# Kernel optimization log

Hardware: AMD Instinct MI355X
Metric: run time of the kernel (lower is better)

## Reference

```python
import jax, jax.numpy as jnp
import numpy as np

K = 7  # local_kernel_size


def conv2d(x, w, b, pad):
    # x: [B,C,H,W], w: [O,I,kh,kw]
    y = jax.lax.conv_general_dilated(
        x, w, window_strides=(1, 1), padding=[(pad, pad), (pad, pad)],
        dimension_numbers=("NCHW", "OIHW", "NCHW"))
    return y + b[None, :, None, None]


def kernel_normalize(kernel, k):
    # kernel: [B, k*k, H, W]; zero-mean over tap dim, then add 1/(k*k)
    km = jnp.mean(kernel, axis=1, keepdims=True)
    return kernel - km + 1.0 / (k * k)


def local_conv_feat(img, kernel, k):
    # Fused dynamic local conv: avoids materializing [B,C,k*k,H,W].
    # Tap order matches F.unfold row-major (dy, dx).
    B, C, H, W = img.shape
    pad = (k - 1) // 2
    imgp = jnp.pad(img, ((0, 0), (0, 0), (pad, pad), (pad, pad)))
    out = jnp.zeros_like(img)
    for dy in range(k):
        for dx in range(k):
            idx = dy * k + dx
            out = out + imgp[:, :, dy:dy + H, dx:dx + W] * kernel[:, idx:idx + 1]
    return out


def setup_inputs() -> dict:
    key = jax.random.key(0)
    ks = jax.random.split(key, 14)
    B, C, H, W = 4, 64, 128, 128
    w = lambda k, shape: jax.random.normal(k, shape, jnp.float32) * 0.05
    return {
        "x": jax.random.normal(ks[0], (B, C, H, W), jnp.float32),
        "kernel_features": jax.random.normal(ks[1], (B, C, H, W), jnp.float32),
        # feature_path: two 3x3 convs
        "fw1": w(ks[2], (C, C, 3, 3)), "fb1": jnp.zeros((C,), jnp.float32),
        "fw2": w(ks[3], (C, C, 3, 3)), "fb2": jnp.zeros((C,), jnp.float32),
        # multiplicative_path: two 3x3 convs
        "mw1": w(ks[4], (C, C, 3, 3)), "mb1": jnp.zeros((C,), jnp.float32),
        "mw2": w(ks[5], (C, C, 3, 3)), "mb2": jnp.zeros((C,), jnp.float32),
        # local_filter_path: two 1x1 convs, last outputs k*k channels
        "lw1": w(ks[6], (C, C, 1, 1)), "lb1": jnp.zeros((C,), jnp.float32),
        "lw2": w(ks[7], (K * K, C, 1, 1)), "lb2": jnp.zeros((K * K,), jnp.float32),
    }


def reference(x, kernel_features, fw1, fb1, fw2, fb2, mw1, mb1, mw2, mb2, lw1, lb1, lw2, lb2):
    # feature_path: ReLU -> conv3x3 -> ReLU -> conv3x3
    fp = conv2d(jax.nn.relu(conv2d(jax.nn.relu(x), fw1, fb1, 1)), fw2, fb2, 1)
    # multiplicative_path: conv3x3 -> ReLU -> conv3x3
    mp = conv2d(jax.nn.relu(conv2d(kernel_features, mw1, mb1, 1)), mw2, mb2, 1)
    # local_filter_path: conv1x1 -> ReLU -> conv1x1 (-> k*k channels)
    lp = conv2d(jax.nn.relu(conv2d(kernel_features, lw1, lb1, 0)), lw2, lb2, 0)
    lp = kernel_normalize(lp, K)
    feat = fp * mp
    filtered = local_conv_feat(feat, lp, K)
    return x + filtered
```

## Files before the change

### kernel.cpp

```cpp
#include <hip/hip_runtime.h>
#include <hip/hip_bf16.h>

#define Cc 64
#define Hc 128
#define Wc 128
#define HWc (Hc * Wc)
#define Bc 4

typedef __attribute__((ext_vector_type(8))) short short8;
typedef __attribute__((ext_vector_type(4))) float float4v;

static __device__ __forceinline__ unsigned short f2bu(float f) {
    __hip_bfloat16 h = __float2bfloat16(f);
    return *(unsigned short*)&h;
}

static __device__ __forceinline__ void gl_lds16(const void* g, void* l) {
    __builtin_amdgcn_global_load_lds(
        (const __attribute__((address_space(1))) unsigned int*)g,
        (__attribute__((address_space(3))) unsigned int*)l, 16, 0, 0);
}

__global__ __launch_bounds__(256) void prep_k(
    const float* __restrict__ x, const float* __restrict__ kf,
    const float* __restrict__ fw1, const float* __restrict__ fw2,
    const float* __restrict__ mw1, const float* __restrict__ mw2,
    const float* __restrict__ lw1, const float* __restrict__ lw2,
    unsigned short* __restrict__ xb, unsigned short* __restrict__ kfb,
    unsigned short* __restrict__ wbase)
{
    const int bid = blockIdx.x;
    const int tid = threadIdx.x;

    if (bid < 512) {
        const bool isx = bid < 256;
        const float* src = isx ? x : kf;
        unsigned short* dst = isx ? xb : kfb;
        const int px = (isx ? bid : bid - 256) * 256 + tid;
        const int b  = px >> 14;
        const int hw = px & 16383;
        const float* s = src + (size_t)b * Cc * HWc + hw;
        unsigned short* d = dst + (size_t)px * Cc;
#pragma unroll
        for (int c8 = 0; c8 < 8; ++c8) {
            unsigned int pk[4];
#pragma unroll
            for (int jp = 0; jp < 4; ++jp) {
                float v0 = s[(size_t)(c8 * 8 + jp * 2 + 0) * HWc];
                float v1 = s[(size_t)(c8 * 8 + jp * 2 + 1) * HWc];
                if (isx) { v0 = fmaxf(v0, 0.f); v1 = fmaxf(v1, 0.f); }
                pk[jp] = (unsigned int)f2bu(v0) | ((unsigned int)f2bu(v1) << 16);
            }
            *(uint4*)(d + c8 * 8) = make_uint4(pk[0], pk[1], pk[2], pk[3]);
        }
    } else if (bid < 584) {
        const int wbid  = bid - 512;
        const int which = wbid / 18;
        const float* w = (which == 0) ? fw1 : (which == 1) ? fw2 : (which == 2) ? mw1 : mw2;
        unsigned short* wb = wbase + (size_t)which * 36864;
        const int g = (wbid % 18) * 256 + tid;
        if (g >= 4608) return;
        const int lane = g & 63;
        const int smt  = g >> 6;
        const int s    = smt >> 2;
        const int mt   = smt & 3;
        const int co   = mt * 16 + (lane & 15);
        const int kb   = s * 32 + (lane >> 4) * 8;
        unsigned int pk[4];
#pragma unroll
        for (int jp = 0; jp < 4; ++jp) {
            int k0 = kb + jp * 2, k1 = k0 + 1;
            float v0 = w[((size_t)co * Cc + (k0 & 63)) * 9 + (k0 >> 6)];
            float v1 = w[((size_t)co * Cc + (k1 & 63)) * 9 + (k1 >> 6)];
            pk[jp] = (unsigned int)f2bu(v0) | ((unsigned int)f2bu(v1) << 16);
        }
        *(uint4*)(wb + (size_t)g * 8) = make_uint4(pk[0], pk[1], pk[2], pk[3]);
    } else {
        const int wbid  = bid - 584;
        const int which = wbid >> 1;
        const float* w = which ? lw2 : lw1;
        const int Cout = which ? 49 : 64;
        unsigned short* wb = wbase + 4 * 36864 + (size_t)which * 4096;
        const int g = (wbid & 1) * 256 + tid;
        const int lane = g & 63;
        const int smt  = g >> 6;
        const int s    = smt >> 2;
        const int mt   = smt & 3;
        const int co   = mt * 16 + (lane & 15);
        const int kb   = s * 32 + (lane >> 4) * 8;
        unsigned int pk[4];
#pragma unroll
        for (int jp = 0; jp < 4; ++jp) {
            int k0 = kb + jp * 2, k1 = k0 + 1;
            float v0 = (co < Cout) ? w[(size_t)co * Cc + k0] : 0.f;
            float v1 = (co < Cout) ? w[(size_t)co * Cc + k1] : 0.f;
            pk[jp] = (unsigned int)f2bu(v0) | ((unsigned int)f2bu(v1) << 16);
        }
        *(uint4*)(wb + (size_t)g * 8) = make_uint4(pk[0], pk[1], pk[2], pk[3]);
    }
}

#define STAGE_DMA(INPTR, SBUF)                                                \
    for (int k = wv; k < 33; k += 4) {                                        \
        const int u_  = k * 8 + (lane >> 3);                                  \
        const int j_  = lane & 7;                                             \
        const int r_  = u_ / 66;                                              \
        const int c_  = u_ - r_ * 66;                                         \
        const int gh_ = h0 - 1 + r_;                                          \
        const int gw_ = w0 - 1 + c_;                                          \
        const bool ok_ = ((unsigned)gh_ < (unsigned)Hc) && ((unsigned)gw_ < (unsigned)Wc); \
        const int ch_ = j_ ^ (u_ & 7);                                        \
        const unsigned short* g_ = ok_                                        \
            ? (INPTR) + ((((size_t)b * Hc + gh_) * Wc + gw_) << 6) + (ch_ << 3) \
            : zpage + (ch_ << 3);                                             \
        gl_lds16(g_, &(SBUF)[k * 512]);                                       \
    }

#define LOAD_A(W, s, m) (*(const short8*)((W) + (size_t)(s) * 2048 + (size_t)(m) * 512))
#define LOAD_B(SB, s, nt) ({                                                  \
        const int tap_ = (s) >> 1;                                            \
        const int qb_  = rowb[tap_ / 3] + tap_ % 3;                           \
        const int ch0_ = ((s) & 1) * 4 + quad;                                \
        *(const short8*)&(SB)[(qb_ + (nt) * 16) * 64 + ((ch0_ ^ (qb_ & 7)) << 3)]; })

#define CONV_GEMM(APTR, ACC, SB)                                              \
    {                                                                         \
        short8 a_cur[2], b_cur[4];                                            \
        _Pragma("unroll")                                                     \
        for (int m = 0; m < 2; ++m) a_cur[m] = LOAD_A(APTR, 0, m);            \
        _Pragma("unroll")                                                     \
        for (int nt = 0; nt < 4; ++nt) b_cur[nt] = LOAD_B(SB, 0, nt);         \
        _Pragma("unroll")                                                     \
        for (int s = 0; s < 18; ++s) {                                        \
            short8 a_nxt[2], b_nxt[4];                                        \
            if (s < 17) {                                                     \
                _Pragma("unroll")                                             \
                for (int m = 0; m < 2; ++m) a_nxt[m] = LOAD_A(APTR, s + 1, m);\
                _Pragma("unroll")                                             \
                for (int nt = 0; nt < 4; ++nt) b_nxt[nt] = LOAD_B(SB, s + 1, nt); \
            }                                                                 \
            _Pragma("unroll")                                                 \
            for (int nt = 0; nt < 4; ++nt)                                    \
                _Pragma("unroll")                                             \
                for (int m = 0; m < 2; ++m)                                   \
                    ACC[m][nt] = __builtin_amdgcn_mfma_f32_16x16x32_bf16(     \
                        a_cur[m], b_cur[nt], ACC[m][nt], 0, 0, 0);            \
            if (s < 17) {                                                     \
                _Pragma("unroll")                                             \
                for (int m = 0; m < 2; ++m) a_cur[m] = a_nxt[m];              \
                _Pragma("unroll")                                             \
                for (int nt = 0; nt < 4; ++nt) b_cur[nt] = b_nxt[nt];         \
            }                                                                 \
        }                                                                     \
    }

__global__ __launch_bounds__(256) void conv1_dual_k(
    const unsigned short* __restrict__ in0,
    const unsigned short* __restrict__ in1,
    const unsigned short* __restrict__ wfrag0,
    const unsigned short* __restrict__ wfrag1,
    const float* __restrict__ bias0,
    const float* __restrict__ bias1,
    const unsigned short* __restrict__ zpage,
    unsigned short* __restrict__ out0,
    unsigned short* __restrict__ out1)
{
    __shared__ unsigned short s_b[264 * 64];

    const int tid  = threadIdx.x;
    const int lane = tid & 63;
    const int wv   = tid >> 6;
    const int w0   = blockIdx.x * 64;
    const int h0   = blockIdx.y * 2;
    const int zz   = blockIdx.z;
    const int b    = zz & 3;
    const bool sel = zz >> 2;

    const unsigned short* in    = sel ? in1 : in0;
    const unsigned short* wfrag = sel ? wfrag1 : wfrag0;
    const float*          bias  = sel ? bias1 : bias0;
    unsigned short*       out   = sel ? out1 : out0;

    STAGE_DMA(in, s_b);
    __syncthreads();

    const int rowsel = wv >> 1;
    const int cohalf = wv & 1;
    const int quad   = lane >> 4;
    const int n15    = lane & 15;
    const unsigned short* aptr = wfrag + (((size_t)(cohalf * 2) * 64 + lane) << 3);

    int rowb[3];
#pragma unroll
    for (int ky = 0; ky < 3; ++ky) rowb[ky] = (rowsel + ky) * 66 + n15;

    float4v acc[2][4];
#pragma unroll
    for (int m = 0; m < 2; ++m)
#pragma unroll
        for (int nt = 0; nt < 4; ++nt) acc[m][nt] = (float4v){0.f, 0.f, 0.f, 0.f};

    CONV_GEMM(aptr, acc, s_b);

    const int h = h0 + rowsel;
#pragma unroll
    for (int m = 0; m < 2; ++m) {
        const int mt  = cohalf * 2 + m;
        const int co0 = mt * 16 + quad * 4;
        float4 bv = *(const float4*)&bias[co0];
#pragma unroll
        for (int nt = 0; nt < 4; ++nt) {
            const size_t pix = ((size_t)b * Hc + h) * Wc + w0 + nt * 16 + n15;
            ushort4 pk;
            pk.x = f2bu(fmaxf(acc[m][nt][0] + bv.x, 0.f));
            pk.y = f2bu(fmaxf(acc[m][nt][1] + bv.y, 0.f));
            pk.z = f2bu(fmaxf(acc[m][nt][2] + bv.z, 0.f));
            pk.w = f2bu(fmaxf(acc[m][nt][3] + bv.w, 0.f));
            *(ushort4*)&out[pix * Cc + co0] = pk;
        }
    }
}

__global__ __launch_bounds__(256) void conv2_fused_k(
    const unsigned short* __restrict__ t1f,
    const unsigned short* __restrict__ t1m,
    const unsigned short* __restrict__ wf,
    const unsigned short* __restrict__ wm,
    const float* __restrict__ bf,
    const float* __restrict__ bm,
    const unsigned short* __restrict__ zpage,
    float* __restrict__ feat)
{
    __shared__ unsigned short s_b2[2][264 * 64];

    const int tid  = threadIdx.x;
    const int lane = tid & 63;
    const int wv   = tid >> 6;
    const int w0   = blockIdx.x * 64;
    const int h0   = blockIdx.y * 2;
    const int b    = blockIdx.z;

    STAGE_DMA(t1f, s_b2[0]);
    STAGE_DMA(t1m, s_b2[1]);
    __syncthreads();

    const int rowsel = wv >> 1;
    const int cohalf = wv & 1;
    const int quad   = lane >> 4;
    const int n15    = lane & 15;

    int rowb[3];
#pragma unroll
    for (int ky = 0; ky < 3; ++ky) rowb[ky] = (rowsel + ky) * 66 + n15;

    float4v acc[2][4];
#pragma unroll
    for (int m = 0; m < 2; ++m)
#pragma unroll
        for (int nt = 0; nt < 4; ++nt) acc[m][nt] = (float4v){0.f, 0.f, 0.f, 0.f};

    {
        const unsigned short* aptr = wf + (((size_t)(cohalf * 2) * 64 + lane) << 3);
        CONV_GEMM(aptr, acc, s_b2[0]);
    }

    unsigned int fpk[2][4][2];
#pragma unroll
    for (int m = 0; m < 2; ++m) {
        const int mt  = cohalf * 2 + m;
        const int co0 = mt * 16 + quad * 4;
        float4 bv = *(const float4*)&bf[co0];
#pragma unroll
        for (int nt = 0; nt < 4; ++nt) {
            fpk[m][nt][0] = (unsigned int)f2bu(acc[m][nt][0] + bv.x)
                          | ((unsigned int)f2bu(acc[m][nt][1] + bv.y) << 16);
            fpk[m][nt][1] = (unsigned int)f2bu(acc[m][nt][2] + bv.z)
                          | ((unsigned int)f2bu(acc[m][nt][3] + bv.w) << 16);
        }
    }

#pragma unroll
    for (int m = 0; m < 2; ++m)
#pragma unroll
        for (int nt = 0; nt < 4; ++nt) acc[m][nt] = (float4v){0.f, 0.f, 0.f, 0.f};

    {
        const unsigned short* aptr = wm + (((size_t)(cohalf * 2) * 64 + lane) << 3);
        CONV_GEMM(aptr, acc, s_b2[1]);
    }

    const int h = h0 + rowsel;
#pragma unroll
    for (int m = 0; m < 2; ++m) {
        const int mt  = cohalf * 2 + m;
        const int co0 = mt * 16 + quad * 4;
        float4 bv = *(const float4*)&bm[co0];
#pragma unroll
        for (int nt = 0; nt < 4; ++nt) {
            float v[4] = {acc[m][nt][0] + bv.x, acc[m][nt][1] + bv.y,
                          acc[m][nt][2] + bv.z, acc[m][nt][3] + bv.w};
            v[0] *= __uint_as_float((fpk[m][nt][0] & 0xffffu) << 16);
            v[1] *= __uint_as_float(fpk[m][nt][0] & 0xffff0000u);
            v[2] *= __uint_as_float((fpk[m][nt][1] & 0xffffu) << 16);
            v[3] *= __uint_as_float(fpk[m][nt][1] & 0xffff0000u);
#pragma unroll
            for (int r = 0; r < 4; ++r)
                feat[((size_t)b * Cc + co0 + r) * HWc + (size_t)h * Wc + w0 + nt * 16 + n15] = v[r];
        }
    }
}

__global__ __launch_bounds__(256) void lp_fused_k(
    const unsigned short* __restrict__ in,
    const unsigned short* __restrict__ w1,
    const float* __restrict__ b1,
    const unsigned short* __restrict__ w2,
    const float* __restrict__ b2,
    float* __restrict__ out)
{
    __shared__ unsigned short s_t[4 * 1024];

    const int tid  = threadIdx.x;
    const int lane = tid & 63;
    const int wv   = tid >> 6;
    const int quad = lane >> 4;
    const int p    = lane & 15;
    const size_t pix = (size_t)blockIdx.x * 64 + wv * 16 + p;
    unsigned short* st = &s_t[wv * 1024];

    float4v acc1[4];
#pragma unroll
    for (int mt = 0; mt < 4; ++mt) acc1[mt] = (float4v){0.f, 0.f, 0.f, 0.f};
#pragma unroll
    for (int s = 0; s < 2; ++s) {
        short8 bfr = *(const short8*)&in[pix * Cc + s * 32 + quad * 8];
#pragma unroll
        for (int mt = 0; mt < 4; ++mt) {
            short8 afr = *(const short8*)&w1[(size_t)(((s * 4 + mt) << 6) + lane) << 3];
            acc1[mt] = __builtin_amdgcn_mfma_f32_16x16x32_bf16(afr, bfr, acc1[mt], 0, 0, 0);
        }
    }

#pragma unroll
    for (int mt = 0; mt < 4; ++mt) {
        const int co0 = mt * 16 + quad * 4;
        float4 bv = *(const float4*)&b1[co0];
        ushort4 pk;
        pk.x = f2bu(fmaxf(acc1[mt][0] + bv.x, 0.f));
        pk.y = f2bu(fmaxf(acc1[mt][1] + bv.y, 0.f));
        pk.z = f2bu(fmaxf(acc1[mt][2] + bv.z, 0.f));
        pk.w = f2bu(fmaxf(acc1[mt][3] + bv.w, 0.f));
        const int cg = co0 >> 3;
        *(ushort4*)&st[p * 64 + ((cg ^ (p & 7)) << 3) + (quad & 1) * 4] = pk;
    }
    __syncthreads();

    float4v acc2[4];
#pragma unroll
    for (int mt = 0; mt < 4; ++mt) acc2[mt] = (float4v){0.f, 0.f, 0.f, 0.f};
#pragma unroll
    for (int s = 0; s < 2; ++s) {
        const int cg = s * 4 + quad;
        short8 bfr = *(const short8*)&st[p * 64 + ((cg ^ (p & 7)) << 3)];
#pragma unroll
        for (int mt = 0; mt < 4; ++mt) {
            short8 afr = *(const short8*)&w2[(size_t)(((s * 4 + mt) << 6) + lane) << 3];
            acc2[mt] = __builtin_amdgcn_mfma_f32_16x16x32_bf16(afr, bfr, acc2[mt], 0, 0, 0);
        }
    }

    float v[4][4];
    float partial = 0.f;
#pragma unroll
    for (int mt = 0; mt < 4; ++mt) {
#pragma unroll
        for (int r = 0; r < 4; ++r) {
            const int tap = mt * 16 + quad * 4 + r;
            float val = (tap < 49) ? (acc2[mt][r] + b2[tap]) : 0.f;
            v[mt][r] = val;
            partial += val;
        }
    }
    partial += __shfl_xor(partial, 16, 64);
    partial += __shfl_xor(partial, 32, 64);
    const float m = partial * (1.f / 49.f) - (1.f / 49.f);

    const int b  = (int)(pix >> 14);
    const int hw = (int)(pix & 16383);
#pragma unroll
    for (int mt = 0; mt < 4; ++mt) {
#pragma unroll
        for (int r = 0; r < 4; ++r) {
            const int tap = mt * 16 + quad * 4 + r;
            if (tap < 49)
                out[((size_t)b * 49 + tap) * HWc + hw] = v[mt][r] - m;
        }
    }
}

__global__ __launch_bounds__(256) void local_conv_v2(
    const float* __restrict__ x, const float* __restrict__ feat,
    const float* __restrict__ lp, float* __restrict__ out)
{
    const int tid = threadIdx.x;
    const int w4  = (tid & 31) * 4;
    const int ro  = tid >> 5;
    const int h   = blockIdx.y * 8 + ro;
    const int c0  = blockIdx.x * 4;
    const int b   = blockIdx.z;

    float msk[12];
#pragma unroll
    for (int e = 0; e < 12; ++e) {
        int gw = w4 - 4 + e;
        msk[e] = ((unsigned)gw < (unsigned)Wc) ? 1.f : 0.f;
    }

    float acc[4][4];
#pragma unroll
    for (int ch = 0; ch < 4; ++ch)
#pragma unroll
        for (int p = 0; p < 4; ++p) acc[ch][p] = 0.f;

    const float* lpb = lp + (size_t)b * 49 * HWc + (size_t)h * Wc + w4;
    const float* fb  = feat + ((size_t)b * Cc + c0) * HWc;

#pragma unroll
    for (int dy = 0; dy < 7; ++dy) {
        const int gh = h + dy - 3;
        if ((unsigned)gh >= (unsigned)Hc) continue;

        float4 lp4[7];
#pragma unroll
        for (int dx = 0; dx < 7; ++dx)
            lp4[dx] = *(const float4*)&lpb[(size_t)(dy * 7 + dx) * HWc];

        const float* frow = fb + (size_t)gh * Wc + w4;
#pragma unroll
        for (int ch = 0; ch < 4; ++ch) {
            const float* fr = frow + (size_t)ch * HWc;
            float4 a  = *(const float4*)(fr - 4);
            float4 bq = *(const float4*)(fr);
            float4 cq = *(const float4*)(fr + 4);
            float f[12];
            f[0]  = a.x;            f[1]  = a.y * msk[1];
            f[2]  = a.z * msk[2];   f[3]  = a.w * msk[3];
            f[4]  = bq.x;           f[5]  = bq.y;
            f[6]  = bq.z;           f[7]  = bq.w;
            f[8]  = cq.x * msk[8];  f[9]  = cq.y * msk[9];
            f[10] = cq.z * msk[10]; f[11] = cq.w;
#pragma unroll
            for (int dx = 0; dx < 7; ++dx) {
                const float* lpv = (const float*)&lp4[dx];
#pragma unroll
                for (int p = 0; p < 4; ++p)
                    acc[ch][p] = fmaf(f[p + dx + 1], lpv[p], acc[ch][p]);
            }
        }
    }

#pragma unroll
    for (int ch = 0; ch < 4; ++ch) {
        const size_t idx = ((size_t)b * Cc + c0 + ch) * HWc + (size_t)h * Wc + w4;
        float4 xv = *(const float4*)&x[idx];
        float4 r  = {acc[ch][0] + xv.x, acc[ch][1] + xv.y,
                     acc[ch][2] + xv.z, acc[ch][3] + xv.w};
        *(float4*)&out[idx] = r;
    }
}

extern "C" void kernel_launch(void* const* d_in, const int* in_sizes, int n_in,
                              void* d_out, int out_size, void* d_ws, size_t ws_size,
                              hipStream_t stream)
{
    const float* x   = (const float*)d_in[0];
    const float* kf  = (const float*)d_in[1];
    const float* fw1 = (const float*)d_in[2];
    const float* fb1 = (const float*)d_in[3];
    const float* fw2 = (const float*)d_in[4];
    const float* fb2 = (const float*)d_in[5];
    const float* mw1 = (const float*)d_in[6];
    const float* mb1 = (const float*)d_in[7];
    const float* mw2 = (const float*)d_in[8];
    const float* mb2 = (const float*)d_in[9];
    const float* lw1 = (const float*)d_in[10];
    const float* lb1 = (const float*)d_in[11];
    const float* lw2 = (const float*)d_in[12];
    const float* lb2 = (const float*)d_in[13];

    float* out = (float*)d_out;
    char*  ws  = (char*)d_ws;

    const size_t NBH = (size_t)Bc * HWc * Cc * 2;
    const size_t NBF = (size_t)Bc * Cc * HWc * 4;
    const size_t LPB = (size_t)Bc * 49 * HWc * 4;
    const size_t WBA = (size_t)(4 * 36864 + 2 * 4096) * 2;

    unsigned short* t1f   = (unsigned short*)(ws);
    unsigned short* t1m   = (unsigned short*)(ws + NBH);
    float*          feat  = (float*)(ws + 2 * NBH);
    float*          lpb   = (float*)(ws + 2 * NBH + NBF);
    unsigned short* xb    = (unsigned short*)(ws + 2 * NBH + NBF + LPB);
    unsigned short* kfb   = (unsigned short*)((char*)xb + NBH);
    unsigned short* wbase = (unsigned short*)((char*)kfb + NBH);
    unsigned short* zpage = (unsigned short*)((char*)wbase + WBA);
    unsigned short* wb1   = wbase;
    unsigned short* wb2   = wbase + 36864;
    unsigned short* wb3   = wbase + 2 * 36864;
    unsigned short* wb4   = wbase + 3 * 36864;
    unsigned short* wl1   = wbase + 4 * 36864;
    unsigned short* wl2   = wbase + 4 * 36864 + 4096;

    dim3 blk(256);
    dim3 gm2(Wc / 64, Hc / 2, Bc * 2);
    dim3 gm (Wc / 64, Hc / 2, Bc);
    dim3 gp (Bc * HWc / 64);
    dim3 glc(Cc / 4, Hc / 8, Bc);

    hipMemsetAsync(zpage, 0, 256, stream);

    prep_k<<<dim3(588), blk, 0, stream>>>(x, kf, fw1, fw2, mw1, mw2, lw1, lw2,
                                          xb, kfb, wbase);

    conv1_dual_k<<<gm2, blk, 0, stream>>>(xb, kfb, wb1, wb3, fb1, mb1, zpage, t1f, t1m);

    conv2_fused_k<<<gm, blk, 0, stream>>>(t1f, t1m, wb2, wb4, fb2, mb2, zpage, feat);

    lp_fused_k<<<gp, blk, 0, stream>>>(kfb, wl1, lb1, wl2, lb2, lpb);

    local_conv_v2<<<glc, blk, 0, stream>>>(x, feat, lpb, out);
}
```

Baseline: 180.2 us.

## Merge local-filter 1x1 path into conv1 launch and deepen weight prefetch

```diff
diff --git a/kernel.cpp b/kernel.cpp
--- a/kernel.cpp
+++ b/kernel.cpp
@@ -125,36 +125,39 @@
 
 #define CONV_GEMM(APTR, ACC, SB)                                              \
     {                                                                         \
-        short8 a_cur[2], b_cur[4];                                            \
+        short8 a_buf[4][2], b_cur[4], b_nxt[4];                               \
         _Pragma("unroll")                                                     \
-        for (int m = 0; m < 2; ++m) a_cur[m] = LOAD_A(APTR, 0, m);            \
+        for (int q = 0; q < 3; ++q)                                           \
+            _Pragma("unroll")                                                 \
+            for (int m = 0; m < 2; ++m) a_buf[q][m] = LOAD_A(APTR, q, m);     \
         _Pragma("unroll")                                                     \
         for (int nt = 0; nt < 4; ++nt) b_cur[nt] = LOAD_B(SB, 0, nt);         \
         _Pragma("unroll")                                                     \
         for (int s = 0; s < 18; ++s) {                                        \
-            short8 a_nxt[2], b_nxt[4];                                        \
-            if (s < 17) {                                                     \
+            if (s + 3 < 18) {                                                 \
                 _Pragma("unroll")                                             \
-                for (int m = 0; m < 2; ++m) a_nxt[m] = LOAD_A(APTR, s + 1, m);\
+                for (int m = 0; m < 2; ++m)                                   \
+                    a_buf[(s + 3) & 3][m] = LOAD_A(APTR, s + 3, m);           \
+            }                                                                 \
+            if (s + 1 < 18) {                                                 \
                 _Pragma("unroll")                                             \
-                for (int nt = 0; nt < 4; ++nt) b_nxt[nt] = LOAD_B(SB, s + 1, nt); \
+                for (int nt = 0; nt < 4; ++nt)                                \
+                    b_nxt[nt] = LOAD_B(SB, s + 1, nt);                        \
             }                                                                 \
             _Pragma("unroll")                                                 \
             for (int nt = 0; nt < 4; ++nt)                                    \
                 _Pragma("unroll")                                             \
                 for (int m = 0; m < 2; ++m)                                   \
                     ACC[m][nt] = __builtin_amdgcn_mfma_f32_16x16x32_bf16(     \
-                        a_cur[m], b_cur[nt], ACC[m][nt], 0, 0, 0);            \
-            if (s < 17) {                                                     \
-                _Pragma("unroll")                                             \
-                for (int m = 0; m < 2; ++m) a_cur[m] = a_nxt[m];              \
+                        a_buf[s & 3][m], b_cur[nt], ACC[m][nt], 0, 0, 0);     \
+            if (s + 1 < 18) {                                                 \
                 _Pragma("unroll")                                             \
                 for (int nt = 0; nt < 4; ++nt) b_cur[nt] = b_nxt[nt];         \
             }                                                                 \
         }                                                                     \
     }
 
-__global__ __launch_bounds__(256) void conv1_dual_k(
+__global__ __launch_bounds__(256) void conv1_lp_k(
     const unsigned short* __restrict__ in0,
     const unsigned short* __restrict__ in1,
     const unsigned short* __restrict__ wfrag0,
@@ -163,60 +166,140 @@
     const float* __restrict__ bias1,
     const unsigned short* __restrict__ zpage,
     unsigned short* __restrict__ out0,
-    unsigned short* __restrict__ out1)
+    unsigned short* __restrict__ out1,
+    const unsigned short* __restrict__ w1, const float* __restrict__ b1,
+    const unsigned short* __restrict__ w2, const float* __restrict__ b2,
+    float* __restrict__ lpout)
 {
     __shared__ unsigned short s_b[264 * 64];
 
     const int tid  = threadIdx.x;
     const int lane = tid & 63;
     const int wv   = tid >> 6;
-    const int w0   = blockIdx.x * 64;
-    const int h0   = blockIdx.y * 2;
+    const int quad = lane >> 4;
     const int zz   = blockIdx.z;
-    const int b    = zz & 3;
-    const bool sel = zz >> 2;
-
-    const unsigned short* in    = sel ? in1 : in0;
-    const unsigned short* wfrag = sel ? wfrag1 : wfrag0;
-    const float*          bias  = sel ? bias1 : bias0;
-    unsigned short*       out   = sel ? out1 : out0;
-
-    STAGE_DMA(in, s_b);
-    __syncthreads();
-
-    const int rowsel = wv >> 1;
-    const int cohalf = wv & 1;
-    const int quad   = lane >> 4;
-    const int n15    = lane & 15;
-    const unsigned short* aptr = wfrag + (((size_t)(cohalf * 2) * 64 + lane) << 3);
-
-    int rowb[3];
-#pragma unroll
-    for (int ky = 0; ky < 3; ++ky) rowb[ky] = (rowsel + ky) * 66 + n15;
-
-    float4v acc[2][4];
-#pragma unroll
-    for (int m = 0; m < 2; ++m)
-#pragma unroll
-        for (int nt = 0; nt < 4; ++nt) acc[m][nt] = (float4v){0.f, 0.f, 0.f, 0.f};
-
-    CONV_GEMM(aptr, acc, s_b);
-
-    const int h = h0 + rowsel;
-#pragma unroll
-    for (int m = 0; m < 2; ++m) {
-        const int mt  = cohalf * 2 + m;
-        const int co0 = mt * 16 + quad * 4;
-        float4 bv = *(const float4*)&bias[co0];
-#pragma unroll
-        for (int nt = 0; nt < 4; ++nt) {
-            const size_t pix = ((size_t)b * Hc + h) * Wc + w0 + nt * 16 + n15;
+
+    if (zz < 8) {
+        const int w0   = blockIdx.x * 64;
+        const int h0   = blockIdx.y * 2;
+        const int b    = zz & 3;
+        const bool sel = zz >> 2;
+
+        const unsigned short* in    = sel ? in1 : in0;
+        const unsigned short* wfrag = sel ? wfrag1 : wfrag0;
+        const float*          bias  = sel ? bias1 : bias0;
+        unsigned short*       out   = sel ? out1 : out0;
+
+        STAGE_DMA(in, s_b);
+        __syncthreads();
+
+        const int rowsel = wv >> 1;
+        const int cohalf = wv & 1;
+        const int n15    = lane & 15;
+        const unsigned short* aptr = wfrag + (((size_t)(cohalf * 2) * 64 + lane) << 3);
+
+        int rowb[3];
+#pragma unroll
+        for (int ky = 0; ky < 3; ++ky) rowb[ky] = (rowsel + ky) * 66 + n15;
+
+        float4v acc[2][4];
+#pragma unroll
+        for (int m = 0; m < 2; ++m)
+#pragma unroll
+            for (int nt = 0; nt < 4; ++nt) acc[m][nt] = (float4v){0.f, 0.f, 0.f, 0.f};
+
+        CONV_GEMM(aptr, acc, s_b);
+
+        const int h = h0 + rowsel;
+#pragma unroll
+        for (int m = 0; m < 2; ++m) {
+            const int mt  = cohalf * 2 + m;
+            const int co0 = mt * 16 + quad * 4;
+            float4 bv = *(const float4*)&bias[co0];
+#pragma unroll
+            for (int nt = 0; nt < 4; ++nt) {
+                const size_t pix = ((size_t)b * Hc + h) * Wc + w0 + nt * 16 + n15;
+                ushort4 pk;
+                pk.x = f2bu(fmaxf(acc[m][nt][0] + bv.x, 0.f));
+                pk.y = f2bu(fmaxf(acc[m][nt][1] + bv.y, 0.f));
+                pk.z = f2bu(fmaxf(acc[m][nt][2] + bv.z, 0.f));
+                pk.w = f2bu(fmaxf(acc[m][nt][3] + bv.w, 0.f));
+                *(ushort4*)&out[pix * Cc + co0] = pk;
+            }
+        }
+    } else {
+        const int lpid = (zz - 8) * 128 + blockIdx.y * 2 + blockIdx.x;
+        const int p    = lane & 15;
+        const size_t pix = (size_t)lpid * 64 + wv * 16 + p;
+        unsigned short* st = &s_b[wv * 1024];
+
+        float4v acc1[4];
+#pragma unroll
+        for (int mt = 0; mt < 4; ++mt) acc1[mt] = (float4v){0.f, 0.f, 0.f, 0.f};
+#pragma unroll
+        for (int s = 0; s < 2; ++s) {
+            short8 bfr = *(const short8*)&in1[pix * Cc + s * 32 + quad * 8];
+#pragma unroll
+            for (int mt = 0; mt < 4; ++mt) {
+                short8 afr = *(const short8*)&w1[(size_t)(((s * 4 + mt) << 6) + lane) << 3];
+                acc1[mt] = __builtin_amdgcn_mfma_f32_16x16x32_bf16(afr, bfr, acc1[mt], 0, 0, 0);
+            }
+        }
+
+#pragma unroll
+        for (int mt = 0; mt < 4; ++mt) {
+            const int co0 = mt * 16 + quad * 4;
+            float4 bv = *(const float4*)&b1[co0];
             ushort4 pk;
-            pk.x = f2bu(fmaxf(acc[m][nt][0] + bv.x, 0.f));
-            pk.y = f2bu(fmaxf(acc[m][nt][1] + bv.y, 0.f));
-            pk.z = f2bu(fmaxf(acc[m][nt][2] + bv.z, 0.f));
-            pk.w = f2bu(fmaxf(acc[m][nt][3] + bv.w, 0.f));
-            *(ushort4*)&out[pix * Cc + co0] = pk;
+            pk.x = f2bu(fmaxf(acc1[mt][0] + bv.x, 0.f));
+            pk.y = f2bu(fmaxf(acc1[mt][1] + bv.y, 0.f));
+            pk.z = f2bu(fmaxf(acc1[mt][2] + bv.z, 0.f));
+            pk.w = f2bu(fmaxf(acc1[mt][3] + bv.w, 0.f));
+            const int cg = co0 >> 3;
+            *(ushort4*)&st[p * 64 + ((cg ^ (p & 7)) << 3) + (quad & 1) * 4] = pk;
+        }
+        __syncthreads();
+
+        float4v acc2[4];
+#pragma unroll
+        for (int mt = 0; mt < 4; ++mt) acc2[mt] = (float4v){0.f, 0.f, 0.f, 0.f};
+#pragma unroll
+        for (int s = 0; s < 2; ++s) {
+            const int cg = s * 4 + quad;
+            short8 bfr = *(const short8*)&st[p * 64 + ((cg ^ (p & 7)) << 3)];
+#pragma unroll
+            for (int mt = 0; mt < 4; ++mt) {
+                short8 afr = *(const short8*)&w2[(size_t)(((s * 4 + mt) << 6) + lane) << 3];
+                acc2[mt] = __builtin_amdgcn_mfma_f32_16x16x32_bf16(afr, bfr, acc2[mt], 0, 0, 0);
+            }
+        }
+
+        float v[4][4];
+        float partial = 0.f;
+#pragma unroll
+        for (int mt = 0; mt < 4; ++mt) {
+#pragma unroll
+            for (int r = 0; r < 4; ++r) {
+                const int tap = mt * 16 + quad * 4 + r;
+                float val = (tap < 49) ? (acc2[mt][r] + b2[tap]) : 0.f;
+                v[mt][r] = val;
+                partial += val;
+            }
+        }
+        partial += __shfl_xor(partial, 16, 64);
+        partial += __shfl_xor(partial, 32, 64);
+        const float m = partial * (1.f / 49.f) - (1.f / 49.f);
+
+        const int b  = (int)(pix >> 14);
+        const int hw = (int)(pix & 16383);
+#pragma unroll
+        for (int mt = 0; mt < 4; ++mt) {
+#pragma unroll
+            for (int r = 0; r < 4; ++r) {
+                const int tap = mt * 16 + quad * 4 + r;
+                if (tap < 49)
+                    lpout[((size_t)b * 49 + tap) * HWc + hw] = v[mt][r] - m;
+            }
         }
     }
 }
@@ -306,94 +389,6 @@
 #pragma unroll
             for (int r = 0; r < 4; ++r)
                 feat[((size_t)b * Cc + co0 + r) * HWc + (size_t)h * Wc + w0 + nt * 16 + n15] = v[r];
-        }
-    }
-}
-
-__global__ __launch_bounds__(256) void lp_fused_k(
-    const unsigned short* __restrict__ in,
-    const unsigned short* __restrict__ w1,
-    const float* __restrict__ b1,
-    const unsigned short* __restrict__ w2,
-    const float* __restrict__ b2,
-    float* __restrict__ out)
-{
-    __shared__ unsigned short s_t[4 * 1024];
-
-    const int tid  = threadIdx.x;
-    const int lane = tid & 63;
-    const int wv   = tid >> 6;
-    const int quad = lane >> 4;
-    const int p    = lane & 15;
-    const size_t pix = (size_t)blockIdx.x * 64 + wv * 16 + p;
-    unsigned short* st = &s_t[wv * 1024];
-
-    float4v acc1[4];
-#pragma unroll
-    for (int mt = 0; mt < 4; ++mt) acc1[mt] = (float4v){0.f, 0.f, 0.f, 0.f};
-#pragma unroll
-    for (int s = 0; s < 2; ++s) {
-        short8 bfr = *(const short8*)&in[pix * Cc + s * 32 + quad * 8];
-#pragma unroll
-        for (int mt = 0; mt < 4; ++mt) {
-            short8 afr = *(const short8*)&w1[(size_t)(((s * 4 + mt) << 6) + lane) << 3];
-            acc1[mt] = __builtin_amdgcn_mfma_f32_16x16x32_bf16(afr, bfr, acc1[mt], 0, 0, 0);
-        }
-    }
-
-#pragma unroll
-    for (int mt = 0; mt < 4; ++mt) {
-        const int co0 = mt * 16 + quad * 4;
-        float4 bv = *(const float4*)&b1[co0];
-        ushort4 pk;
-        pk.x = f2bu(fmaxf(acc1[mt][0] + bv.x, 0.f));
-        pk.y = f2bu(fmaxf(acc1[mt][1] + bv.y, 0.f));
-        pk.z = f2bu(fmaxf(acc1[mt][2] + bv.z, 0.f));
-        pk.w = f2bu(fmaxf(acc1[mt][3] + bv.w, 0.f));
-        const int cg = co0 >> 3;
-        *(ushort4*)&st[p * 64 + ((cg ^ (p & 7)) << 3) + (quad & 1) * 4] = pk;
-    }
-    __syncthreads();
-
-    float4v acc2[4];
-#pragma unroll
-    for (int mt = 0; mt < 4; ++mt) acc2[mt] = (float4v){0.f, 0.f, 0.f, 0.f};
-#pragma unroll
-    for (int s = 0; s < 2; ++s) {
-        const int cg = s * 4 + quad;
-        short8 bfr = *(const short8*)&st[p * 64 + ((cg ^ (p & 7)) << 3)];
-#pragma unroll
-        for (int mt = 0; mt < 4; ++mt) {
-            short8 afr = *(const short8*)&w2[(size_t)(((s * 4 + mt) << 6) + lane) << 3];
-            acc2[mt] = __builtin_amdgcn_mfma_f32_16x16x32_bf16(afr, bfr, acc2[mt], 0, 0, 0);
-        }
-    }
-
-    float v[4][4];
-    float partial = 0.f;
-#pragma unroll
-    for (int mt = 0; mt < 4; ++mt) {
-#pragma unroll
-        for (int r = 0; r < 4; ++r) {
-            const int tap = mt * 16 + quad * 4 + r;
-            float val = (tap < 49) ? (acc2[mt][r] + b2[tap]) : 0.f;
-            v[mt][r] = val;
-            partial += val;
-        }
-    }
-    partial += __shfl_xor(partial, 16, 64);
-    partial += __shfl_xor(partial, 32, 64);
-    const float m = partial * (1.f / 49.f) - (1.f / 49.f);
-
-    const int b  = (int)(pix >> 14);
-    const int hw = (int)(pix & 16383);
-#pragma unroll
-    for (int mt = 0; mt < 4; ++mt) {
-#pragma unroll
-        for (int r = 0; r < 4; ++r) {
-            const int tap = mt * 16 + quad * 4 + r;
-            if (tap < 49)
-                out[((size_t)b * 49 + tap) * HWc + hw] = v[mt][r] - m;
         }
     }
 }
@@ -512,9 +507,8 @@
     unsigned short* wl2   = wbase + 4 * 36864 + 4096;
 
     dim3 blk(256);
-    dim3 gm2(Wc / 64, Hc / 2, Bc * 2);
+    dim3 gc1(Wc / 64, Hc / 2, 16);
     dim3 gm (Wc / 64, Hc / 2, Bc);
-    dim3 gp (Bc * HWc / 64);
     dim3 glc(Cc / 4, Hc / 8, Bc);
 
     hipMemsetAsync(zpage, 0, 256, stream);
@@ -522,11 +516,10 @@
     prep_k<<<dim3(588), blk, 0, stream>>>(x, kf, fw1, fw2, mw1, mw2, lw1, lw2,
                                           xb, kfb, wbase);
 
-    conv1_dual_k<<<gm2, blk, 0, stream>>>(xb, kfb, wb1, wb3, fb1, mb1, zpage, t1f, t1m);
+    conv1_lp_k<<<gc1, blk, 0, stream>>>(xb, kfb, wb1, wb3, fb1, mb1, zpage,
+                                        t1f, t1m, wl1, lb1, wl2, lb2, lpb);
 
     conv2_fused_k<<<gm, blk, 0, stream>>>(t1f, t1m, wb2, wb4, fb2, mb2, zpage, feat);
 
-    lp_fused_k<<<gp, blk, 0, stream>>>(kfb, wl1, lb1, wl2, lb2, lpb);
-
     local_conv_v2<<<glc, blk, 0, stream>>>(x, feat, lpb, out);
 }
```

New measurement: 178.6 us. No clear change (-0.9%).
